# Performance work log

Hardware: AMD Instinct MI355X
Metric: run time of the kernel (lower is better)

The kernel has to match this reference:

```python
import jax, jax.numpy as jnp
import numpy as np

KK_THRESHOLD = 1000.0

def setup_inputs() -> dict:
    key = jax.random.key(0)
    k1, k2 = jax.random.split(key)
    x = jax.random.normal(k1, (8192, 4096), dtype=jnp.float32)
    # kernel initialized Uniform(-0.1, 0.1) as in the original layer
    kernel = jax.random.uniform(k2, (4096, 4096), dtype=jnp.float32, minval=-0.1, maxval=0.1)
    bias = jnp.zeros((4096,), dtype=jnp.float32)
    nmk = jnp.float32(1.0)
    kk = jnp.float32(1.0)  # < 1000 -> soft tanh quantization branch
    return {"x": x, "kernel": kernel, "bias": bias, "nmk": nmk, "kk": kk}

def reference(x, kernel, bias, nmk, kk):
    def soft(_):
        # training-time soft binarization: tanh(kk * W)
        return nmk * jnp.matmul(x, jnp.tanh(kernel * kk)) + bias
    def hard(_):
        # fully binarized: sign(W)
        return nmk * jnp.matmul(x, jnp.sign(kernel)) + bias
    return jax.lax.cond(kk < KK_THRESHOLD, soft, hard, operand=None)
```

## Files before the change

### kernel.cpp

```cpp
#include <hip/hip_runtime.h>
#include <hip/hip_bf16.h>
#include <stdint.h>

typedef __bf16 bf16x8 __attribute__((ext_vector_type(8)));
typedef float f32x4 __attribute__((ext_vector_type(4)));
typedef unsigned int u32;
typedef __attribute__((address_space(1))) const u32 g_u32;
typedef __attribute__((address_space(3))) u32 l_u32;

__device__ __forceinline__ unsigned short f32_bf16_rne(float f) {
    unsigned u = __float_as_uint(f);
    u += 0x7FFFu + ((u >> 16) & 1u);
    return (unsigned short)(u >> 16);
}

__device__ __forceinline__ void lds16(const void* g, void* l) {
    __builtin_amdgcn_global_load_lds((g_u32*)g, (l_u32*)l, 16, 0, 0);
}

__global__ void conv_x(const float* __restrict__ x, unsigned short* __restrict__ xb, int n8) {
    int i = blockIdx.x * blockDim.x + threadIdx.x;
    if (i >= n8) return;
    const float4* p = (const float4*)x + (size_t)i * 2;
    float4 a = p[0];
    float4 b = p[1];
    union { unsigned short u[8]; uint4 v; } o;
    o.u[0] = f32_bf16_rne(a.x); o.u[1] = f32_bf16_rne(a.y);
    o.u[2] = f32_bf16_rne(a.z); o.u[3] = f32_bf16_rne(a.w);
    o.u[4] = f32_bf16_rne(b.x); o.u[5] = f32_bf16_rne(b.y);
    o.u[6] = f32_bf16_rne(b.z); o.u[7] = f32_bf16_rne(b.w);
    *((uint4*)xb + i) = o.v;
}

__global__ __launch_bounds__(256) void quant_transpose(
    const float* __restrict__ W, unsigned short* __restrict__ Wt,
    const float* __restrict__ kk_p, int K, int N)
{
    __shared__ unsigned short tileT[64][66];
    const float kk = *kk_p;
    const bool soft = kk < 1000.0f;
    const int kb = blockIdx.y * 64;
    const int nb = blockIdx.x * 64;
    const int t = threadIdx.x;

#pragma unroll
    for (int j = 0; j < 4; ++j) {
        const int r  = j * 16 + (t >> 4);
        const int c4 = (t & 15) * 4;
        float4 w = *(const float4*)&W[(size_t)(kb + r) * N + nb + c4];
        float q0, q1, q2, q3;
        if (soft) {
            q0 = tanhf(w.x * kk); q1 = tanhf(w.y * kk);
            q2 = tanhf(w.z * kk); q3 = tanhf(w.w * kk);
        } else {
            q0 = (w.x > 0.f) ? 1.f : (w.x < 0.f ? -1.f : 0.f);
            q1 = (w.y > 0.f) ? 1.f : (w.y < 0.f ? -1.f : 0.f);
            q2 = (w.z > 0.f) ? 1.f : (w.z < 0.f ? -1.f : 0.f);
            q3 = (w.w > 0.f) ? 1.f : (w.w < 0.f ? -1.f : 0.f);
        }
        tileT[c4 + 0][r] = f32_bf16_rne(q0);
        tileT[c4 + 1][r] = f32_bf16_rne(q1);
        tileT[c4 + 2][r] = f32_bf16_rne(q2);
        tileT[c4 + 3][r] = f32_bf16_rne(q3);
    }
    __syncthreads();
#pragma unroll
    for (int j = 0; j < 2; ++j) {
        const int n = j * 32 + (t >> 3);
        const int c = (t & 7) * 8;
        uint4 v;
        v.x = *(const u32*)&tileT[n][c + 0];
        v.y = *(const u32*)&tileT[n][c + 2];
        v.z = *(const u32*)&tileT[n][c + 4];
        v.w = *(const u32*)&tileT[n][c + 6];
        *(uint4*)&Wt[(size_t)(nb + n) * K + kb + c] = v;
    }
}

__global__ __launch_bounds__(256) void gemm_bf16_bt(
    const unsigned short* __restrict__ A,
    const unsigned short* __restrict__ Bt,
    const float* __restrict__ bias,
    const float* __restrict__ nmk_p,
    float* __restrict__ C,
    int M, int N, int K)
{
    __shared__ __align__(16) unsigned short As[128 * 32];
    __shared__ __align__(16) unsigned short Bs[128 * 32];

    const int tid  = threadIdx.x;
    const int wave = tid >> 6;
    const int lane = tid & 63;
    const int mTile = blockIdx.y * 128;
    const int nTile = blockIdx.x * 128;
    const int wm = (wave & 1) * 64;
    const int wn = (wave >> 1) * 64;
    const int lr = lane & 15;

    f32x4 acc[4][4] = {};

    const int srow = tid >> 2;
    const int scol = (((tid & 3) ^ ((srow >> 1) & 3))) * 8;
    const unsigned short* Ag0 = A  + (size_t)(mTile + srow) * K + scol;
    const unsigned short* Ag1 = Ag0 + (size_t)64 * K;
    const unsigned short* Bg0 = Bt + (size_t)(nTile + srow) * K + scol;
    const unsigned short* Bg1 = Bg0 + (size_t)64 * K;

    char* asw = (char*)As + wave * 1024;
    char* bsw = (char*)Bs + wave * 1024;

    const int sw16 = (((lane >> 4) ^ ((lr >> 1) & 3))) * 16;

    for (int k0 = 0; k0 < K; k0 += 32) {
        __syncthreads();
        lds16(Ag0, asw);
        lds16(Ag1, asw + 4096);
        lds16(Bg0, bsw);
        lds16(Bg1, bsw + 4096);
        Ag0 += 32; Ag1 += 32; Bg0 += 32; Bg1 += 32;
        __syncthreads();

        bf16x8 af[4], bf[4];
#pragma unroll
        for (int mi = 0; mi < 4; ++mi)
            af[mi] = *(const bf16x8*)((const char*)As + (wm + 16 * mi + lr) * 64 + sw16);
#pragma unroll
        for (int ni = 0; ni < 4; ++ni)
            bf[ni] = *(const bf16x8*)((const char*)Bs + (wn + 16 * ni + lr) * 64 + sw16);
#pragma unroll
        for (int mi = 0; mi < 4; ++mi)
#pragma unroll
            for (int ni = 0; ni < 4; ++ni)
                acc[mi][ni] = __builtin_amdgcn_mfma_f32_16x16x32_bf16(
                    af[mi], bf[ni], acc[mi][ni], 0, 0, 0);
    }

    const float nmk = *nmk_p;
    float bn[4];
#pragma unroll
    for (int ni = 0; ni < 4; ++ni) bn[ni] = bias[nTile + wn + 16 * ni + lr];

#pragma unroll
    for (int mi = 0; mi < 4; ++mi) {
        const int m0 = mTile + wm + 16 * mi + (lane >> 4) * 4;
#pragma unroll
        for (int ni = 0; ni < 4; ++ni) {
            const int n = nTile + wn + 16 * ni + lr;
            float* cp = C + (size_t)m0 * N + n;
#pragma unroll
            for (int r = 0; r < 4; ++r)
                cp[(size_t)r * N] = nmk * acc[mi][ni][r] + bn[ni];
        }
    }
}

__global__ void fallback_gemm(const float* __restrict__ x, const float* __restrict__ W,
                              const float* __restrict__ bias, const float* __restrict__ nmk_p,
                              const float* __restrict__ kk_p, float* __restrict__ C,
                              int M, int N, int K) {
    __shared__ float At[16][17];
    __shared__ float Bq[16][17];
    const int tx = threadIdx.x, ty = threadIdx.y;
    const int n = blockIdx.x * 16 + tx;
    const int m = blockIdx.y * 16 + ty;
    const float kk = *kk_p;
    const bool soft = kk < 1000.f;
    float acc = 0.f;
    for (int k0 = 0; k0 < K; k0 += 16) {
        At[ty][tx] = x[(size_t)m * K + k0 + tx];
        float w = W[(size_t)(k0 + ty) * N + n];
        Bq[ty][tx] = soft ? tanhf(w * kk) : (w > 0.f ? 1.f : (w < 0.f ? -1.f : 0.f));
        __syncthreads();
#pragma unroll
        for (int kk2 = 0; kk2 < 16; ++kk2) acc += At[ty][kk2] * Bq[kk2][tx];
        __syncthreads();
    }
    C[(size_t)m * N + n] = (*nmk_p) * acc + bias[n];
}

extern "C" void kernel_launch(void* const* d_in, const int* in_sizes, int n_in,
                              void* d_out, int out_size, void* d_ws, size_t ws_size,
                              hipStream_t stream) {
    const float* x    = (const float*)d_in[0];
    const float* W    = (const float*)d_in[1];
    const float* bias = (const float*)d_in[2];
    const float* nmk  = (const float*)d_in[3];
    const float* kk   = (const float*)d_in[4];
    float* out = (float*)d_out;

    const int N = in_sizes[2];
    const int K = in_sizes[1] / N;
    const int M = in_sizes[0] / K;

    const size_t need = ((size_t)M * K + (size_t)N * K) * sizeof(unsigned short);
    const bool shapes_ok = (M % 128 == 0) && (N % 128 == 0) && (K % 64 == 0) &&
                           (N % 64 == 0) && ((M * K) % 2048 == 0);

    if (ws_size >= need && shapes_ok) {
        unsigned short* xb = (unsigned short*)d_ws;
        unsigned short* Wt = xb + (size_t)M * K;

        const int n8 = (M * K) / 8;
        conv_x<<<(n8 + 255) / 256, 256, 0, stream>>>(x, xb, n8);

        dim3 qg(N / 64, K / 64);
        quant_transpose<<<qg, 256, 0, stream>>>(W, Wt, kk, K, N);

        dim3 gg(N / 128, M / 128);
        gemm_bf16_bt<<<gg, 256, 0, stream>>>(xb, Wt, bias, nmk, out, M, N, K);
    } else {
        dim3 fg(N / 16, M / 16);
        fallback_gemm<<<fg, dim3(16, 16), 0, stream>>>(x, W, bias, nmk, kk, out, M, N, K);
    }
}
```

Baseline: 605.6 us.

## Use 32x32x16 MFMA in GEMM and fuse prep kernels into one launch

Replaces the 16x16x32 bf16 MFMA tiling with 32x32x16 MFMAs: each wave now holds 2x2 accumulators of 16 floats and reads two k-halves per stage, which cuts LDS fragment loads per MFMA. The x-to-bf16 conversion and the weight quantize-transpose are merged into a single launch, removing one kernel launch and letting the two preparation jobs overlap. tanhf is replaced with an exp-based fast tanh, which is less accurate and may lose precision near zero, though bf16 rounding likely hides this. The epilogue store pattern changes to match the 32x32 accumulator layout.

```diff
diff --git a/kernel.cpp b/kernel.cpp
--- a/kernel.cpp
+++ b/kernel.cpp
@@ -3,7 +3,7 @@
 #include <stdint.h>
 
 typedef __bf16 bf16x8 __attribute__((ext_vector_type(8)));
-typedef float f32x4 __attribute__((ext_vector_type(4)));
+typedef float f32x16 __attribute__((ext_vector_type(16)));
 typedef unsigned int u32;
 typedef __attribute__((address_space(1))) const u32 g_u32;
 typedef __attribute__((address_space(3))) u32 l_u32;
@@ -14,66 +14,70 @@
     return (unsigned short)(u >> 16);
 }
 
+__device__ __forceinline__ float fast_tanh(float z) {
+    return 1.0f - 2.0f / (1.0f + __expf(2.0f * z));
+}
+
 __device__ __forceinline__ void lds16(const void* g, void* l) {
     __builtin_amdgcn_global_load_lds((g_u32*)g, (l_u32*)l, 16, 0, 0);
 }
 
-__global__ void conv_x(const float* __restrict__ x, unsigned short* __restrict__ xb, int n8) {
-    int i = blockIdx.x * blockDim.x + threadIdx.x;
-    if (i >= n8) return;
-    const float4* p = (const float4*)x + (size_t)i * 2;
-    float4 a = p[0];
-    float4 b = p[1];
-    union { unsigned short u[8]; uint4 v; } o;
-    o.u[0] = f32_bf16_rne(a.x); o.u[1] = f32_bf16_rne(a.y);
-    o.u[2] = f32_bf16_rne(a.z); o.u[3] = f32_bf16_rne(a.w);
-    o.u[4] = f32_bf16_rne(b.x); o.u[5] = f32_bf16_rne(b.y);
-    o.u[6] = f32_bf16_rne(b.z); o.u[7] = f32_bf16_rne(b.w);
-    *((uint4*)xb + i) = o.v;
-}
-
-__global__ __launch_bounds__(256) void quant_transpose(
+__global__ __launch_bounds__(256) void prep(
+    const float* __restrict__ x, unsigned short* __restrict__ xb, int n8,
     const float* __restrict__ W, unsigned short* __restrict__ Wt,
-    const float* __restrict__ kk_p, int K, int N)
+    const float* __restrict__ kk_p, int K, int N, int qbx, int qblocks)
 {
-    __shared__ unsigned short tileT[64][66];
-    const float kk = *kk_p;
-    const bool soft = kk < 1000.0f;
-    const int kb = blockIdx.y * 64;
-    const int nb = blockIdx.x * 64;
     const int t = threadIdx.x;
-
-#pragma unroll
-    for (int j = 0; j < 4; ++j) {
-        const int r  = j * 16 + (t >> 4);
-        const int c4 = (t & 15) * 4;
-        float4 w = *(const float4*)&W[(size_t)(kb + r) * N + nb + c4];
-        float q0, q1, q2, q3;
-        if (soft) {
-            q0 = tanhf(w.x * kk); q1 = tanhf(w.y * kk);
-            q2 = tanhf(w.z * kk); q3 = tanhf(w.w * kk);
-        } else {
-            q0 = (w.x > 0.f) ? 1.f : (w.x < 0.f ? -1.f : 0.f);
-            q1 = (w.y > 0.f) ? 1.f : (w.y < 0.f ? -1.f : 0.f);
-            q2 = (w.z > 0.f) ? 1.f : (w.z < 0.f ? -1.f : 0.f);
-            q3 = (w.w > 0.f) ? 1.f : (w.w < 0.f ? -1.f : 0.f);
-        }
-        tileT[c4 + 0][r] = f32_bf16_rne(q0);
-        tileT[c4 + 1][r] = f32_bf16_rne(q1);
-        tileT[c4 + 2][r] = f32_bf16_rne(q2);
-        tileT[c4 + 3][r] = f32_bf16_rne(q3);
-    }
-    __syncthreads();
-#pragma unroll
-    for (int j = 0; j < 2; ++j) {
-        const int n = j * 32 + (t >> 3);
-        const int c = (t & 7) * 8;
-        uint4 v;
-        v.x = *(const u32*)&tileT[n][c + 0];
-        v.y = *(const u32*)&tileT[n][c + 2];
-        v.z = *(const u32*)&tileT[n][c + 4];
-        v.w = *(const u32*)&tileT[n][c + 6];
-        *(uint4*)&Wt[(size_t)(nb + n) * K + kb + c] = v;
+    if ((int)blockIdx.x < qblocks) {
+        __shared__ unsigned short tileT[64][66];
+        const float kk = *kk_p;
+        const bool soft = kk < 1000.0f;
+        const int nb = (blockIdx.x % qbx) * 64;
+        const int kb = (blockIdx.x / qbx) * 64;
+#pragma unroll
+        for (int j = 0; j < 4; ++j) {
+            const int r  = j * 16 + (t >> 4);
+            const int c4 = (t & 15) * 4;
+            float4 w = *(const float4*)&W[(size_t)(kb + r) * N + nb + c4];
+            float q0, q1, q2, q3;
+            if (soft) {
+                q0 = fast_tanh(w.x * kk); q1 = fast_tanh(w.y * kk);
+                q2 = fast_tanh(w.z * kk); q3 = fast_tanh(w.w * kk);
+            } else {
+                q0 = (w.x > 0.f) ? 1.f : (w.x < 0.f ? -1.f : 0.f);
+                q1 = (w.y > 0.f) ? 1.f : (w.y < 0.f ? -1.f : 0.f);
+                q2 = (w.z > 0.f) ? 1.f : (w.z < 0.f ? -1.f : 0.f);
+                q3 = (w.w > 0.f) ? 1.f : (w.w < 0.f ? -1.f : 0.f);
+            }
+            tileT[c4 + 0][r] = f32_bf16_rne(q0);
+            tileT[c4 + 1][r] = f32_bf16_rne(q1);
+            tileT[c4 + 2][r] = f32_bf16_rne(q2);
+            tileT[c4 + 3][r] = f32_bf16_rne(q3);
+        }
+        __syncthreads();
+#pragma unroll
+        for (int j = 0; j < 2; ++j) {
+            const int n = j * 32 + (t >> 3);
+            const int c = (t & 7) * 8;
+            uint4 v;
+            v.x = *(const u32*)&tileT[n][c + 0];
+            v.y = *(const u32*)&tileT[n][c + 2];
+            v.z = *(const u32*)&tileT[n][c + 4];
+            v.w = *(const u32*)&tileT[n][c + 6];
+            *(uint4*)&Wt[(size_t)(nb + n) * K + kb + c] = v;
+        }
+    } else {
+        const int i = ((int)blockIdx.x - qblocks) * 256 + t;
+        if (i >= n8) return;
+        const float4* p = (const float4*)x + (size_t)i * 2;
+        float4 a = p[0];
+        float4 b = p[1];
+        union { unsigned short u[8]; uint4 v; } o;
+        o.u[0] = f32_bf16_rne(a.x); o.u[1] = f32_bf16_rne(a.y);
+        o.u[2] = f32_bf16_rne(a.z); o.u[3] = f32_bf16_rne(a.w);
+        o.u[4] = f32_bf16_rne(b.x); o.u[5] = f32_bf16_rne(b.y);
+        o.u[6] = f32_bf16_rne(b.z); o.u[7] = f32_bf16_rne(b.w);
+        *((uint4*)xb + i) = o.v;
     }
 }
 
@@ -95,9 +99,10 @@
     const int nTile = blockIdx.x * 128;
     const int wm = (wave & 1) * 64;
     const int wn = (wave >> 1) * 64;
-    const int lr = lane & 15;
-
-    f32x4 acc[4][4] = {};
+    const int lm = lane & 31;
+    const int half = lane >> 5;
+
+    f32x16 acc[2][2] = {};
 
     const int srow = tid >> 2;
     const int scol = (((tid & 3) ^ ((srow >> 1) & 3))) * 8;
@@ -109,7 +114,8 @@
     char* asw = (char*)As + wave * 1024;
     char* bsw = (char*)Bs + wave * 1024;
 
-    const int sw16 = (((lane >> 4) ^ ((lr >> 1) & 3))) * 16;
+    const int g = (lane >> 1) & 3;
+    const int p0 = (half ^ g) * 16;
 
     for (int k0 = 0; k0 < K; k0 += 32) {
         __syncthreads();
@@ -120,36 +126,45 @@
         Ag0 += 32; Ag1 += 32; Bg0 += 32; Bg1 += 32;
         __syncthreads();
 
-        bf16x8 af[4], bf[4];
-#pragma unroll
-        for (int mi = 0; mi < 4; ++mi)
-            af[mi] = *(const bf16x8*)((const char*)As + (wm + 16 * mi + lr) * 64 + sw16);
-#pragma unroll
-        for (int ni = 0; ni < 4; ++ni)
-            bf[ni] = *(const bf16x8*)((const char*)Bs + (wn + 16 * ni + lr) * 64 + sw16);
-#pragma unroll
-        for (int mi = 0; mi < 4; ++mi)
-#pragma unroll
-            for (int ni = 0; ni < 4; ++ni)
-                acc[mi][ni] = __builtin_amdgcn_mfma_f32_16x16x32_bf16(
-                    af[mi], bf[ni], acc[mi][ni], 0, 0, 0);
+        bf16x8 af[2][2], bf[2][2];
+#pragma unroll
+        for (int mi = 0; mi < 2; ++mi) {
+            const int rb = (wm + 32 * mi + lm) * 64;
+            af[mi][0] = *(const bf16x8*)((const char*)As + rb + p0);
+            af[mi][1] = *(const bf16x8*)((const char*)As + rb + (p0 ^ 32));
+        }
+#pragma unroll
+        for (int ni = 0; ni < 2; ++ni) {
+            const int rb = (wn + 32 * ni + lm) * 64;
+            bf[ni][0] = *(const bf16x8*)((const char*)Bs + rb + p0);
+            bf[ni][1] = *(const bf16x8*)((const char*)Bs + rb + (p0 ^ 32));
+        }
+#pragma unroll
+        for (int ks = 0; ks < 2; ++ks)
+#pragma unroll
+            for (int mi = 0; mi < 2; ++mi)
+#pragma unroll
+                for (int ni = 0; ni < 2; ++ni)
+                    acc[mi][ni] = __builtin_amdgcn_mfma_f32_32x32x16_bf16(
+                        af[mi][ks], bf[ni][ks], acc[mi][ni], 0, 0, 0);
     }
 
     const float nmk = *nmk_p;
-    float bn[4];
-#pragma unroll
-    for (int ni = 0; ni < 4; ++ni) bn[ni] = bias[nTile + wn + 16 * ni + lr];
-
-#pragma unroll
-    for (int mi = 0; mi < 4; ++mi) {
-        const int m0 = mTile + wm + 16 * mi + (lane >> 4) * 4;
-#pragma unroll
-        for (int ni = 0; ni < 4; ++ni) {
-            const int n = nTile + wn + 16 * ni + lr;
-            float* cp = C + (size_t)m0 * N + n;
-#pragma unroll
-            for (int r = 0; r < 4; ++r)
-                cp[(size_t)r * N] = nmk * acc[mi][ni][r] + bn[ni];
+    float bn[2];
+#pragma unroll
+    for (int ni = 0; ni < 2; ++ni) bn[ni] = bias[nTile + wn + 32 * ni + lm];
+
+#pragma unroll
+    for (int mi = 0; mi < 2; ++mi) {
+        const int mbase = mTile + wm + 32 * mi + 4 * half;
+#pragma unroll
+        for (int ni = 0; ni < 2; ++ni) {
+            const int n = nTile + wn + 32 * ni + lm;
+#pragma unroll
+            for (int reg = 0; reg < 16; ++reg) {
+                const int row = mbase + (reg & 3) + 8 * (reg >> 2);
+                C[(size_t)row * N + n] = nmk * acc[mi][ni][reg] + bn[ni];
+            }
         }
     }
 }
@@ -201,10 +216,10 @@
         unsigned short* Wt = xb + (size_t)M * K;
 
         const int n8 = (M * K) / 8;
-        conv_x<<<(n8 + 255) / 256, 256, 0, stream>>>(x, xb, n8);
-
-        dim3 qg(N / 64, K / 64);
-        quant_transpose<<<qg, 256, 0, stream>>>(W, Wt, kk, K, N);
+        const int qbx = N / 64;
+        const int qblocks = qbx * (K / 64);
+        const int cblocks = (n8 + 255) / 256;
+        prep<<<qblocks + cblocks, 256, 0, stream>>>(x, xb, n8, W, Wt, kk, K, N, qbx, qblocks);
 
         dim3 gg(N / 128, M / 128);
         gemm_bf16_bt<<<gg, 256, 0, stream>>>(xb, Wt, bias, nmk, out, M, N, K);
```

Result: faster. 588.5 us (-2.8%).
